# Optimization experiments

Hardware: AMD Instinct MI355X
Metric: run time of the kernel (lower is better)

## Reference

```python
import jax, jax.numpy as jnp
import numpy as np

EPS = 1e-5  # torch InstanceNorm2d default eps


def conv1x1(x, w, b):
    # x: [B,C,H,W], w: [O,C], b: [O]
    return jnp.einsum('bchw,oc->bohw', x, w) + b[None, :, None, None]


def conv3x3(x, w, b):
    y = jax.lax.conv_general_dilated(x, w, (1, 1), 'SAME',
                                     dimension_numbers=('NCHW', 'OIHW', 'NCHW'))
    return y + b[None, :, None, None]


def inorm(x):
    # InstanceNorm2d, affine=False, biased variance
    m = jnp.mean(x, axis=(2, 3), keepdims=True)
    v = jnp.var(x, axis=(2, 3), keepdims=True)
    return (x - m) * jax.lax.rsqrt(v + EPS)


def self_attn(x, wq, bq, wk, bk, wv, bv, gamma):
    B, C, H, W = x.shape
    N = H * W
    q = conv1x1(x, wq, bq).reshape(B, -1, N)   # [B,C/8,N]
    k = conv1x1(x, wk, bk).reshape(B, -1, N)   # [B,C/8,N]
    A = jax.nn.softmax(jnp.einsum('bdn,bdm->bnm', q, k), axis=-1)  # [B,N,N]
    v = conv1x1(x, wv, bv).reshape(B, C, N)    # [B,C,N]
    out = jnp.einsum('bcm,bnm->bcn', v, A).reshape(B, C, H, W)
    return gamma * out + x


def setup_inputs() -> dict:
    key = jax.random.key(0)
    B, C, H, W = 2, 256, 64, 64
    C8 = C // 8
    ks = iter(jax.random.split(key, 40))

    def n(shape, scale=0.05):
        return jax.random.normal(next(ks), shape, dtype=jnp.float32) * scale

    inp = {
        'x': jax.random.normal(next(ks), (B, C, H, W), dtype=jnp.float32),
        'y': jax.random.normal(next(ks), (B, C, H, W), dtype=jnp.float32),
    }
    for p in ('sa1', 'sa2', 'top'):
        inp[p + '_wq'] = n((C8, C)); inp[p + '_bq'] = n((C8,))
        inp[p + '_wk'] = n((C8, C)); inp[p + '_bk'] = n((C8,))
        inp[p + '_wv'] = n((C, C));  inp[p + '_bv'] = n((C,))
        inp[p + '_gamma'] = n((1,), 0.1)
    inp['conv1_w'] = n((C, C, 3, 3)); inp['conv1_b'] = n((C,))
    inp['conv2_w'] = n((C, C, 3, 3)); inp['conv2_b'] = n((C,))
    return inp


def reference(x, y,
              sa1_wq, sa1_bq, sa1_wk, sa1_bk, sa1_wv, sa1_bv, sa1_gamma,
              sa2_wq, sa2_bq, sa2_wk, sa2_bk, sa2_wv, sa2_bv, sa2_gamma,
              top_wq, top_bq, top_wk, top_bk, top_wv, top_bv, top_gamma,
              conv1_w, conv1_b, conv2_w, conv2_b):
    out_1 = inorm(self_attn(x, sa1_wq, sa1_bq, sa1_wk, sa1_bk, sa1_wv, sa1_bv, sa1_gamma))
    out_2 = inorm(out_1 + conv3x3(out_1, conv1_w, conv1_b))
    out_3 = inorm(self_attn(y, sa2_wq, sa2_bq, sa2_wk, sa2_bk, sa2_wv, sa2_bv, sa2_gamma))

    B, C, H, W = out_2.shape
    N = H * W
    q = conv1x1(out_2, top_wq, top_bq).reshape(B, -1, N)
    k = conv1x1(out_2, top_wk, top_bk).reshape(B, -1, N)
    A = jax.nn.softmax(jnp.einsum('bdn,bdm->bnm', q, k), axis=-1)
    v = conv1x1(out_3, top_wv, top_bv).reshape(B, C, N)
    out = jnp.einsum('bcm,bnm->bcn', v, A).reshape(B, C, H, W)
    out = top_gamma * out + y
    out = inorm(out)
    out = inorm(out + out_3)
    out_4 = conv3x3(out, conv2_w, conv2_b)
    out = inorm(out + out_4)
    return out
```

## Files before the change

### kernel.cpp

```cpp
#include <hip/hip_runtime.h>
#include <hip/hip_bf16.h>

typedef __hip_bfloat16 bf16;
typedef __attribute__((ext_vector_type(8))) short s8v;
typedef __attribute__((ext_vector_type(4))) short s4v;
typedef __attribute__((ext_vector_type(4))) float f4v;

#define NPIX 4096
#define CDIM 256
#define MN_ELEMS (1 << 20)
#define QKVSTR (320L * NPIX)
#define QKTSTR (64L * NPIX)

#if __has_builtin(__builtin_amdgcn_exp2f)
#define EXP2F(x) __builtin_amdgcn_exp2f(x)
#else
#define EXP2F(x) exp2f(x)
#endif

typedef __attribute__((address_space(1))) const unsigned int g_u32;
typedef __attribute__((address_space(3))) unsigned int l_u32;
__device__ __forceinline__ void glds16(const void* g, void* l) {
  __builtin_amdgcn_global_load_lds((g_u32*)g, (l_u32*)l, 16, 0, 0);
}

__device__ inline s8v ld8(const bf16* p) { return *(const s8v*)p; }
__device__ inline s8v ld8(const float* p) {
  float4 f0 = *(const float4*)p;
  float4 f1 = *(const float4*)(p + 4);
  s8v r; bf16* e = (bf16*)&r;
  e[0] = __float2bfloat16(f0.x); e[1] = __float2bfloat16(f0.y);
  e[2] = __float2bfloat16(f0.z); e[3] = __float2bfloat16(f0.w);
  e[4] = __float2bfloat16(f1.x); e[5] = __float2bfloat16(f1.y);
  e[6] = __float2bfloat16(f1.z); e[7] = __float2bfloat16(f1.w);
  return r;
}

template<int NT>
__global__ __launch_bounds__(256) void fattn_k(
    const bf16* __restrict__ qkt, const bf16* __restrict__ Vg,
    bf16* __restrict__ out)
{
  constexpr int SN  = NT / 32;
  constexpr int NST = NT / 16;
  __shared__ bf16 k_s[128 * 32];
  __shared__ bf16 p_s[4 * NT * 32];
  float* sums = (float*)k_s;

  const int tid = threadIdx.x;
  const int z = blockIdx.z;
  const int w = tid >> 6, lane = tid & 63;
  const int l15 = lane & 15, oct = lane >> 4;
  const int wr = w >> 1, wc = w & 1;
  const int n0 = blockIdx.x * NT, c0 = blockIdx.y * 128;
  const bf16* qk = qkt + (long)z * QKTSTR;
  const bf16* Vz = Vg + (long)z * QKVSTR;
  const int srow = lane >> 2, scol = (lane & 3) * 8;

  const bf16* vb0 = Vz + (long)(c0 + w * 32 + l15) * 4096 + oct * 8;
  const bf16* vb1 = vb0 + 16L * 4096;

  #pragma unroll
  for (int g = 0; g < NT / 64; ++g)
    glds16(qk + (long)(n0 + g * 64 + (w << 4) + srow) * 64 + scol,
           p_s + g * 2048 + w * 512);
  glds16(qk + (long)((w << 4) + srow) * 64 + 32 + scol, k_s + w * 512);
  glds16(qk + (long)(64 + (w << 4) + srow) * 64 + 32 + scol, k_s + 2048 + w * 512);
  __syncthreads();

  s8v qf[SN];
  #pragma unroll
  for (int st = 0; st < SN; ++st)
    qf[st] = *(const s8v*)(p_s + (wr * (NT / 2) + st * 16 + l15) * 32 + oct * 8);
  __syncthreads();

  f4v acc[2][NST];
  #pragma unroll
  for (int i = 0; i < 2; ++i)
    #pragma unroll
    for (int j = 0; j < NST; ++j) acc[i][j] = (f4v){0.f, 0.f, 0.f, 0.f};
  float rs[SN];
  #pragma unroll
  for (int st = 0; st < SN; ++st) rs[st] = 0.f;

  for (int i = 0; i < 32; ++i) {
    s8v vreg[2][4];
    #pragma unroll
    for (int kk = 0; kk < 4; ++kk) {
      vreg[0][kk] = *(const s8v*)(vb0 + (long)i * 128 + kk * 32);
      vreg[1][kk] = *(const s8v*)(vb1 + (long)i * 128 + kk * 32);
    }
    s8v kf[4];
    #pragma unroll
    for (int nt = 0; nt < 4; ++nt)
      kf[nt] = *(const s8v*)(k_s + (wc * 64 + nt * 16 + l15) * 32 + oct * 8);
    #pragma unroll
    for (int st = 0; st < SN; ++st) {
      const int n = wr * (NT / 2) + st * 16 + l15;
      const int sw = ((n >> 1) & 3) << 4;
      f4v sa[4];
      __builtin_amdgcn_s_setprio(1);
      #pragma unroll
      for (int nt = 0; nt < 4; ++nt) {
        f4v zz = (f4v){0.f, 0.f, 0.f, 0.f};
        sa[nt] = __builtin_amdgcn_mfma_f32_16x16x32_bf16(kf[nt], qf[st], zz, 0, 0, 0);
      }
      __builtin_amdgcn_s_setprio(0);
      #pragma unroll
      for (int nt = 0; nt < 4; ++nt) {
        const int kk = wc * 2 + (nt >> 1);
        int byte = kk * (NT * 64) + n * 64 + (nt & 1) * 32 + oct * 8;
        byte ^= sw;
        s4v pk; bf16* pe = (bf16*)&pk;
        float rsum = 0.f;
        #pragma unroll
        for (int r = 0; r < 4; ++r) {
          float e = EXP2F(sa[nt][r]);
          rsum += e;
          pe[r] = __float2bfloat16(e);
        }
        rs[st] += rsum;
        *(s4v*)((char*)p_s + byte) = pk;
      }
    }
    __syncthreads();
    if (i < 31) {
      const int m1 = (i + 1) * 128;
      glds16(qk + (long)(m1 + (w << 4) + srow) * 64 + 32 + scol, k_s + w * 512);
      glds16(qk + (long)(m1 + 64 + (w << 4) + srow) * 64 + 32 + scol, k_s + 2048 + w * 512);
    }
    #pragma unroll
    for (int kk = 0; kk < 4; ++kk) {
      s8v pf[NST];
      #pragma unroll
      for (int nt = 0; nt < NST; ++nt) {
        const int n = nt * 16 + l15;
        int byte = kk * (NT * 64) + n * 64 + oct * 16;
        byte ^= ((n >> 1) & 3) << 4;
        pf[nt] = *(const s8v*)((const char*)p_s + byte);
      }
      __builtin_amdgcn_s_setprio(1);
      #pragma unroll
      for (int st = 0; st < 2; ++st)
        #pragma unroll
        for (int nt = 0; nt < NST; ++nt)
          acc[st][nt] = __builtin_amdgcn_mfma_f32_16x16x32_bf16(vreg[st][kk], pf[nt], acc[st][nt], 0, 0, 0);
      __builtin_amdgcn_s_setprio(0);
    }
    __syncthreads();
  }

  #pragma unroll
  for (int st = 0; st < SN; ++st) {
    rs[st] += __shfl_xor(rs[st], 16);
    rs[st] += __shfl_xor(rs[st], 32);
  }
  if (lane < 16) {
    #pragma unroll
    for (int st = 0; st < SN; ++st)
      sums[wc * NT + wr * (NT / 2) + st * 16 + l15] = rs[st];
  }
  __syncthreads();

  float rinv[NST];
  #pragma unroll
  for (int nt = 0; nt < NST; ++nt) {
    const int n = nt * 16 + l15;
    rinv[nt] = 1.f / (sums[n] + sums[NT + n]);
  }
  bf16* op = out + (long)z * ((long)CDIM * NPIX);
  #pragma unroll
  for (int st = 0; st < 2; ++st) {
    const int gc = c0 + w * 32 + st * 16 + oct * 4;
    #pragma unroll
    for (int nt = 0; nt < NST; ++nt) {
      const int gn = n0 + nt * 16 + l15;
      #pragma unroll
      for (int r = 0; r < 4; ++r)
        op[(long)(gc + r) * NPIX + gn] = __float2bfloat16(acc[st][nt][r] * rinv[nt]);
    }
  }
}

__global__ __launch_bounds__(256) void gemm128(
    const bf16* __restrict__ A, const bf16* __restrict__ Bm,
    bf16* __restrict__ Cp, int N, int K, int nchunk, int nsplit,
    long abat, long bbat)
{
  __shared__ bf16 a_s0[128 * 32], a_s1[128 * 32];
  __shared__ bf16 b_s0[128 * 32], b_s1[128 * 32];
  const int tid = threadIdx.x;
  const int z = blockIdx.z;
  const int bb = z / nsplit, ks = z - bb * nsplit;
  A  += bb * abat;
  Bm += bb * bbat;
  const int w = tid >> 6, lane = tid & 63;
  const int l15 = lane & 15, oct = lane >> 4;
  const int wr = w >> 1, wc = w & 1;
  const int m0 = blockIdx.y * 128, n0 = blockIdx.x * 128;
  const int kc0 = ks * nchunk, kc1 = kc0 + nchunk;

  const int srow = lane >> 2, skoff = (lane & 3) * 8;
  const long aRow0 = (long)(m0 + (w << 4) + srow) * K;
  const long aRow1 = (long)(m0 + ((w + 4) << 4) + srow) * K;
  const long bRow0 = (long)(n0 + (w << 4) + srow) * K;
  const long bRow1 = (long)(n0 + ((w + 4) << 4) + srow) * K;
  const int ldsOff0 = (w) * 512, ldsOff1 = (w + 4) * 512;

  f4v acc[4][4];
  #pragma unroll
  for (int i = 0; i < 4; ++i)
    #pragma unroll
    for (int j = 0; j < 4; ++j) acc[i][j] = (f4v){0.f, 0.f, 0.f, 0.f};

  for (int kc = kc0; kc < kc1; ++kc) {
    const int kb0 = kc * 64 + skoff;
    const int kb1 = kb0 + 32;
    glds16(A + aRow0 + kb0, a_s0 + ldsOff0);
    glds16(A + aRow1 + kb0, a_s0 + ldsOff1);
    glds16(A + aRow0 + kb1, a_s1 + ldsOff0);
    glds16(A + aRow1 + kb1, a_s1 + ldsOff1);
    glds16(Bm + bRow0 + kb0, b_s0 + ldsOff0);
    glds16(Bm + bRow1 + kb0, b_s0 + ldsOff1);
    glds16(Bm + bRow0 + kb1, b_s1 + ldsOff0);
    glds16(Bm + bRow1 + kb1, b_s1 + ldsOff1);
    __syncthreads();
    #pragma unroll
    for (int h = 0; h < 2; ++h) {
      const bf16* as = h ? a_s1 : a_s0;
      const bf16* bs = h ? b_s1 : b_s0;
      s8v af[4], bfv[4];
      #pragma unroll
      for (int st = 0; st < 4; ++st)
        af[st] = *(const s8v*)(as + (wr * 64 + st * 16 + l15) * 32 + oct * 8);
      #pragma unroll
      for (int nt = 0; nt < 4; ++nt)
        bfv[nt] = *(const s8v*)(bs + (wc * 64 + nt * 16 + l15) * 32 + oct * 8);
      #pragma unroll
      for (int st = 0; st < 4; ++st)
        #pragma unroll
        for (int nt = 0; nt < 4; ++nt)
          acc[st][nt] = __builtin_amdgcn_mfma_f32_16x16x32_bf16(af[st], bfv[nt], acc[st][nt], 0, 0, 0);
    }
    __syncthreads();
  }

  bf16* Cz = Cp + (long)z * ((long)gridDim.y * 128) * N;
  #pragma unroll
  for (int st = 0; st < 4; ++st) {
    const int gm = m0 + wr * 64 + st * 16 + oct * 4;
    #pragma unroll
    for (int nt = 0; nt < 4; ++nt) {
      const int gn = n0 + wc * 64 + nt * 16 + l15;
      #pragma unroll
      for (int r = 0; r < 4; ++r)
        Cz[(long)(gm + r) * N + gn] = __float2bfloat16(acc[st][nt][r]);
    }
  }
}

template<int QKT, typename TBe>
__global__ __launch_bounds__(256) void proj_k(
    const float* __restrict__ A, const float* __restrict__ A2,
    const TBe* __restrict__ B1, const TBe* __restrict__ B2,
    const float* __restrict__ bias, const float* __restrict__ bias2,
    bf16* __restrict__ Cm, bf16* __restrict__ qkt,
    int M, int N, int K, long bbat, long cbat, int nchunk)
{
  __shared__ bf16 a_s[64][40];
  __shared__ bf16 b_s[64][40];
  const int tid = threadIdx.x;
  const int z = blockIdx.z, stage = z >> 1, bat = z & 1;
  const float* Au = stage ? A2 : A;
  const float* biasu = stage ? bias2 : bias;
  const TBe* Bm = (stage ? B2 : B1) + bat * bbat;
  Cm += z * cbat;
  if (QKT) qkt += z * QKTSTR;
  const int m0 = blockIdx.y * 64, n0 = blockIdx.x * 64;
  const int w = tid >> 6, lane = tid & 63;
  const int l15 = lane & 15, oct = lane >> 4;

  f4v acc[4];
  #pragma unroll
  for (int i = 0; i < 4; ++i) acc[i] = (f4v){0.f, 0.f, 0.f, 0.f};

  const int a_i0 = tid >> 2, a_i1 = (tid & 3) * 8;
  const int b_i0 = tid >> 3, b_i1 = (tid & 7) * 8;

  s8v pa, pb;
  auto ldA = [&](int kc, s8v& d) {
    if (m0 + a_i0 < M) d = ld8(Au + (long)(m0 + a_i0) * K + kc * 32 + a_i1);
    else d = (s8v){0,0,0,0,0,0,0,0};
  };
  auto ldB = [&](int kc, s8v& d) {
    d = ld8(Bm + (long)(kc * 32 + b_i0) * N + n0 + b_i1);
  };

  ldA(0, pa); ldB(0, pb);
  for (int kc = 0; kc < nchunk; ++kc) {
    *(s8v*)&a_s[a_i0][a_i1] = pa;
    {
      const bf16* e = (const bf16*)&pb;
      #pragma unroll
      for (int j = 0; j < 8; ++j) b_s[b_i1 + j][b_i0] = e[j];
    }
    __syncthreads();
    if (kc + 1 < nchunk) { ldA(kc + 1, pa); ldB(kc + 1, pb); }
    s8v af = *(const s8v*)&a_s[w * 16 + l15][oct * 8];
    #pragma unroll
    for (int nt = 0; nt < 4; ++nt) {
      s8v bfr = *(const s8v*)&b_s[nt * 16 + l15][oct * 8];
      acc[nt] = __builtin_amdgcn_mfma_f32_16x16x32_bf16(af, bfr, acc[nt], 0, 0, 0);
    }
    __syncthreads();
  }
  const int gm_base = m0 + w * 16 + oct * 4;
  #pragma unroll
  for (int nt = 0; nt < 4; ++nt) {
    const int gn = n0 + nt * 16 + l15;
    #pragma unroll
    for (int r = 0; r < 4; ++r) {
      int gm = gm_base + r;
      if (gm < M) {
        float vv = acc[nt][r] + biasu[gm];
        if (QKT && gm < 64) {
          float vv2 = (gm < 32) ? vv * 1.44269504f : vv;
          qkt[(long)gn * 64 + gm] = __float2bfloat16(vv2);
        } else {
          Cm[(long)gm * N + gn] = __float2bfloat16(vv);
        }
      }
    }
  }
}

__global__ __launch_bounds__(256) void reduce_bias_k(
    const bf16* __restrict__ part, const float* __restrict__ bias,
    bf16* __restrict__ out, int nsplit)
{
  const int g8 = (blockIdx.x * 256 + threadIdx.x) * 8;
  const int b = g8 >> 20, i = g8 & (MN_ELEMS - 1);
  const bf16* p0 = part + (long)b * nsplit * MN_ELEMS + i;
  float s[8];
  { s8v v = *(const s8v*)p0; const bf16* e = (const bf16*)&v;
    #pragma unroll
    for (int j = 0; j < 8; ++j) s[j] = __bfloat162float(e[j]); }
  for (int p = 1; p < nsplit; ++p) {
    s8v v = *(const s8v*)(p0 + (long)p * MN_ELEMS); const bf16* e = (const bf16*)&v;
    #pragma unroll
    for (int j = 0; j < 8; ++j) s[j] += __bfloat162float(e[j]);
  }
  float bv = bias[i >> 12];
  s8v o; bf16* eo = (bf16*)&o;
  #pragma unroll
  for (int j = 0; j < 8; ++j) eo[j] = __float2bfloat16(s[j] + bv);
  *(s8v*)(out + g8) = o;
}

__global__ __launch_bounds__(256) void cat_k(
    const float* __restrict__ wq, const float* __restrict__ bq,
    const float* __restrict__ wk, const float* __restrict__ bk,
    const float* __restrict__ wv, const float* __restrict__ bv,
    float* __restrict__ wcat, float* __restrict__ bcat, int M)
{
  int idx = blockIdx.x * 256 + threadIdx.x;
  int total = M << 8;
  if (idx < total) {
    int r = idx >> 8, c = idx & 255;
    float v;
    if (r < 32) v = wq[r * 256 + c];
    else if (r < 64) v = wk[(r - 32) * 256 + c];
    else v = wv[(r - 64) * 256 + c];
    wcat[idx] = v;
  } else if (idx < total + M) {
    int r = idx - total;
    bcat[r] = (r < 32) ? bq[r] : (r < 64) ? bk[r - 32] : bv[r - 64];
  }
}

__global__ __launch_bounds__(256) void cvtw2_k(
    const float* __restrict__ w1, const float* __restrict__ w2,
    bf16* __restrict__ o1, bf16* __restrict__ o2)
{
  const float* in = blockIdx.y ? w2 : w1;
  bf16* out = blockIdx.y ? o2 : o1;
  int idx = blockIdx.x * 256 + threadIdx.x;
  int o = idx / 2304, r = idx % 2304;
  int j = r >> 8, c = r & 255;
  out[idx] = __float2bfloat16(in[(o * 256 + c) * 9 + j]);
}

__global__ __launch_bounds__(256) void im2colT2_k(const bf16* __restrict__ x,
                                                  bf16* __restrict__ colT)
{
  __shared__ bf16 lds[3 * 66 * 66];
  const int tid = threadIdx.x;
  const int h = blockIdx.x, c0 = blockIdx.y * 64;
  x    += (long)blockIdx.z * CDIM * NPIX;
  colT += (long)blockIdx.z * 2304L * NPIX;

  if (tid < 192) {
    int row = tid >> 6, c = tid & 63;
    lds[(row * 66 + 0) * 66 + c] = __float2bfloat16(0.f);
    lds[(row * 66 + 65) * 66 + c] = __float2bfloat16(0.f);
  }
  const int w2 = tid & 31, chi = tid >> 5;
  #pragma unroll
  for (int it = 0; it < 24; ++it) {
    int row = it >> 3, cg = it & 7;
    int c = cg * 8 + chi;
    int hh = h + row - 1;
    unsigned int pix = 0;
    if ((unsigned)hh < 64u)
      pix = *(const unsigned int*)(x + (long)(c0 + c) * 4096 + hh * 64 + w2 * 2);
    const bf16* pp = (const bf16*)&pix;
    lds[(row * 66 + (w2 * 2 + 1)) * 66 + c] = pp[0];
    lds[(row * 66 + (w2 * 2 + 2)) * 66 + c] = pp[1];
  }
  __syncthreads();
  const int cg8 = tid & 7, wq = tid >> 3;
  #pragma unroll
  for (int j = 0; j < 9; ++j) {
    const int dy = j / 3, dx = j % 3;
    #pragma unroll
    for (int half = 0; half < 2; ++half) {
      int w = wq + half * 32;
      s8v v = *(const s8v*)&lds[(dy * 66 + (w + dx)) * 66 + cg8 * 8];
      *(s8v*)(colT + (long)(h * 64 + w) * 2304 + j * 256 + c0 + cg8 * 8) = v;
    }
  }
}

__device__ inline void ld16(const bf16* p, float* v) {
  s8v r0 = *(const s8v*)p, r1 = *(const s8v*)(p + 8);
  const bf16* e0 = (const bf16*)&r0; const bf16* e1 = (const bf16*)&r1;
  #pragma unroll
  for (int j = 0; j < 8; ++j) { v[j] = __bfloat162float(e0[j]); v[8 + j] = __bfloat162float(e1[j]); }
}
__device__ inline void ld16(const float* p, float* v) {
  #pragma unroll
  for (int q = 0; q < 4; ++q) {
    float4 f = *(const float4*)(p + q * 4);
    v[q * 4 + 0] = f.x; v[q * 4 + 1] = f.y; v[q * 4 + 2] = f.z; v[q * 4 + 3] = f.w;
  }
}
__device__ inline void st16(bf16* p, const float* v) {
  s8v o0, o1v; bf16* f0 = (bf16*)&o0; bf16* f1 = (bf16*)&o1v;
  #pragma unroll
  for (int j = 0; j < 8; ++j) { f0[j] = __float2bfloat16(v[j]); f1[j] = __float2bfloat16(v[8 + j]); }
  *(s8v*)p = o0; *(s8v*)(p + 8) = o1v;
}
__device__ inline void st16(float* p, const float* v) {
  #pragma unroll
  for (int q = 0; q < 4; ++q) {
    float4 f; f.x = v[q * 4 + 0]; f.y = v[q * 4 + 1]; f.z = v[q * 4 + 2]; f.w = v[q * 4 + 3];
    *(float4*)(p + q * 4) = f;
  }
}

template<typename TAe, typename TBe, typename TOe, int G>
__global__ __launch_bounds__(256) void inorm_k(
    const TAe* __restrict__ a, const TBe* __restrict__ b,
    const float* __restrict__ g, TOe* __restrict__ out)
{
  __shared__ float red[8];
  const int tid = threadIdx.x;
  const long base = (long)blockIdx.x * NPIX + tid * 16;
  float gv = G ? *g : 1.f;
  float va[16], vbv[16], v[16];
  ld16(a + base, va);
  ld16(b + base, vbv);
  #pragma unroll
  for (int j = 0; j < 16; ++j) v[j] = gv * va[j] + vbv[j];
  float sum = 0.f, sq = 0.f;
  #pragma unroll
  for (int j = 0; j < 16; ++j) { sum += v[j]; sq += v[j] * v[j]; }
  #pragma unroll
  for (int s = 32; s; s >>= 1) { sum += __shfl_xor(sum, s); sq += __shfl_xor(sq, s); }
  if ((tid & 63) == 0) { red[tid >> 6] = sum; red[4 + (tid >> 6)] = sq; }
  __syncthreads();
  sum = red[0] + red[1] + red[2] + red[3];
  sq  = red[4] + red[5] + red[6] + red[7];
  float mean = sum * (1.f / NPIX);
  float var  = fmaxf(sq * (1.f / NPIX) - mean * mean, 0.f);
  float rstd = rsqrtf(var + 1e-5f);
  float o[16];
  #pragma unroll
  for (int j = 0; j < 16; ++j) o[j] = (v[j] - mean) * rstd;
  st16(out + base, o);
}

static const long CN = (long)CDIM * NPIX;

static void attn_core(int nb, bf16* qkv, bf16* qkt, bf16* t0, hipStream_t stream)
{
  fattn_k<64><<<dim3(64, 2, nb), dim3(256), 0, stream>>>(qkt, qkv + 64 * NPIX, t0);
}

static void run_conv(const bf16* src, const bf16* wcvt, const float* cb,
                     bf16* colT, bf16* part, bf16* dst, hipStream_t stream)
{
  dim3 TB(256);
  im2colT2_k<<<dim3(64, 4, 2), TB, 0, stream>>>(src, colT);
  gemm128<<<dim3(32, 2, 8), TB, 0, stream>>>(wcvt, colT, part, NPIX, 2304, 9, 4,
                                             0L, 2304L * NPIX);
  reduce_bias_k<<<dim3(1024), TB, 0, stream>>>(part, cb, dst, 4);
}

extern "C" void kernel_launch(void* const* d_in, const int* in_sizes, int n_in,
                              void* d_out, int out_size, void* d_ws, size_t ws_size,
                              hipStream_t stream)
{
  (void)in_sizes; (void)n_in; (void)out_size; (void)ws_size;
  const float* x = (const float*)d_in[0];
  const float* y = (const float*)d_in[1];
  auto W = [&](int i) { return (const float*)d_in[i]; };

  char* wp = (char*)d_ws;
  auto take = [&](size_t nbytes) { char* p = wp; wp += (nbytes + 255) & ~(size_t)255; return p; };
  bf16*  qkv   = (bf16*)take((size_t)4 * QKVSTR * 2);
  bf16*  qkt   = (bf16*)take((size_t)4 * QKTSTR * 2);
  bf16*  t0    = (bf16*)take((size_t)4 * CN * 2);
  bf16*  u1    = (bf16*)take(2 * CN * 2);
  bf16*  u2    = (bf16*)take(2 * CN * 2);
  bf16*  u3    = (bf16*)take(2 * CN * 2);
  bf16*  u4    = (bf16*)take(2 * CN * 2);
  bf16*  colT  = (bf16*)take((size_t)2 * 2304L * NPIX * 2);
  bf16*  wcvt1 = (bf16*)take((size_t)589824 * 2);
  bf16*  wcvt2 = (bf16*)take((size_t)589824 * 2);
  float* wcat1 = (float*)take((size_t)81920 * 4);
  float* bcat1 = (float*)take(320 * 4);
  float* wcat2 = (float*)take((size_t)81920 * 4);
  float* bcat2 = (float*)take(320 * 4);
  float* wqk   = (float*)take((size_t)16384 * 4);
  float* bqk   = (float*)take(64 * 4);
  bf16*  part  = (bf16*)take((size_t)8 * MN_ELEMS * 2);
  bf16*  cvout = qkv;

  dim3 TB(256);

  cat_k<<<dim3(322), TB, 0, stream>>>(W(2), W(3), W(4), W(5), W(6), W(7), wcat1, bcat1, 320);
  cat_k<<<dim3(322), TB, 0, stream>>>(W(9), W(10), W(11), W(12), W(13), W(14), wcat2, bcat2, 320);
  cat_k<<<dim3(65),  TB, 0, stream>>>(W(16), W(17), W(18), W(19), nullptr, nullptr, wqk, bqk, 64);
  cvtw2_k<<<dim3(2304, 2), TB, 0, stream>>>(W(23), W(25), wcvt1, wcvt2);

  proj_k<1,float><<<dim3(64,5,4), TB, 0, stream>>>(
      wcat1, wcat2, x, y, bcat1, bcat2, qkv, qkt, 320, NPIX, 256, CN, QKVSTR, 8);
  attn_core(4, qkv, qkt, t0, stream);

  inorm_k<bf16,float,bf16,1><<<dim3(512), TB, 0, stream>>>(t0, x, W(8), u1);
  inorm_k<bf16,float,bf16,1><<<dim3(512), TB, 0, stream>>>(t0 + 2 * CN, y, W(15), u3);

  run_conv(u1, wcvt1, W(24), colT, part, cvout, stream);
  inorm_k<bf16,bf16,bf16,0><<<dim3(512), TB, 0, stream>>>(u1, cvout, nullptr, u2);

  proj_k<1,bf16><<<dim3(64,1,2), TB, 0, stream>>>(
      wqk, wqk, u2, u2, bqk, bqk, qkv, qkt, 64, NPIX, 256, CN, QKVSTR, 8);
  proj_k<0,bf16><<<dim3(64,4,2), TB, 0, stream>>>(
      W(20), W(20), u3, u3, W(21), W(21), qkv + 64 * NPIX, qkt, 256, NPIX, 256, CN, QKVSTR, 8);
  attn_core(2, qkv, qkt, t0, stream);
  inorm_k<bf16,float,bf16,1><<<dim3(512), TB, 0, stream>>>(t0, y, W(22), u1);
  inorm_k<bf16,bf16,bf16,0><<<dim3(512), TB, 0, stream>>>(u1, u3, nullptr, u4);
  run_conv(u4, wcvt2, W(26), colT, part, cvout, stream);
  inorm_k<bf16,bf16,float,0><<<dim3(512), TB, 0, stream>>>(u4, cvout, nullptr, (float*)d_out);
}
```

Before: 399.2 us.

## Restructure flash-attention kernel with per-wave key split and register-resident K/Q fragments

The attention kernel drops the shared-memory staging of Q and K tiles and the block-wide barriers inside the key loop. Each wave now reads its Q and K fragments straight from global memory into registers, double-buffering K across a macro-unrolled pair of steps. Waves split the keys by column half and keep P in a private LDS slab, and the two halves are summed through LDS at the end. The channel tile per block becomes a template parameter chosen by batch count, giving more blocks for the two-batch case. The goal is to remove __syncthreads stalls and LDS traffic, at the cost of more global/L2 loads, higher register pressure and an extra reduction step.

New measurement: 418.4 us. 1.05x slower.

```diff
diff --git a/kernel.cpp b/kernel.cpp
--- a/kernel.cpp
+++ b/kernel.cpp
@@ -36,149 +36,130 @@
   return r;
 }
 
-template<int NT>
+#define ATTN_HALF(I, KFC, KFN)                                                \
+  {                                                                           \
+    s8v vfr[NC][2];                                                           \
+    _Pragma("unroll") for (int cst = 0; cst < NC; ++cst)                      \
+      _Pragma("unroll") for (int b = 0; b < 2; ++b)                           \
+        vfr[cst][b] = *(const s8v*)(vp + (long)cst * 65536 + (long)(I) * 128 + b * 32); \
+    _Pragma("unroll") for (int st = 0; st < 4; ++st) {                        \
+      f4v sa[4];                                                              \
+      __builtin_amdgcn_s_setprio(1);                                          \
+      _Pragma("unroll") for (int nt = 0; nt < 4; ++nt) {                      \
+        f4v zz = (f4v){0.f, 0.f, 0.f, 0.f};                                   \
+        sa[nt] = __builtin_amdgcn_mfma_f32_16x16x32_bf16(KFC[nt], qf[st], zz, 0, 0, 0); \
+      }                                                                       \
+      __builtin_amdgcn_s_setprio(0);                                          \
+      _Pragma("unroll") for (int nt = 0; nt < 4; ++nt) {                      \
+        s4v pk; bf16* pe = (bf16*)&pk;                                        \
+        float rsum = 0.f;                                                     \
+        _Pragma("unroll") for (int r = 0; r < 4; ++r) {                       \
+          float e = EXP2F(sa[nt][r]);                                         \
+          rsum += e; pe[r] = __float2bfloat16(e);                             \
+        }                                                                     \
+        rs[st] += rsum;                                                       \
+        *(s4v*)(slab + ((st * 2 + (nt >> 1)) * 4 + ((nt & 1) * 2 + (oct >> 1))) * 256 \
+                + l15 * 16 + (oct & 1) * 8) = pk;                             \
+      }                                                                       \
+    }                                                                         \
+    { const int inx = ((I) + 1) & 31;                                         \
+      _Pragma("unroll") for (int nt = 0; nt < 4; ++nt)                        \
+        KFN[nt] = *(const s8v*)(kp + (long)inx * 8192 + nt * 1024); }         \
+    _Pragma("unroll") for (int b = 0; b < 2; ++b) {                           \
+      s8v pf[4];                                                              \
+      _Pragma("unroll") for (int st = 0; st < 4; ++st)                        \
+        pf[st] = *(const s8v*)(slab + ((st * 2 + b) * 4 + oct) * 256 + l15 * 16); \
+      __builtin_amdgcn_s_setprio(1);                                          \
+      _Pragma("unroll") for (int cst = 0; cst < NC; ++cst)                    \
+        _Pragma("unroll") for (int st = 0; st < 4; ++st)                      \
+          acc[cst][st] = __builtin_amdgcn_mfma_f32_16x16x32_bf16(vfr[cst][b], pf[st], acc[cst][st], 0, 0, 0); \
+      __builtin_amdgcn_s_setprio(0);                                          \
+    }                                                                         \
+  }
+
+template<int CB>
 __global__ __launch_bounds__(256) void fattn_k(
     const bf16* __restrict__ qkt, const bf16* __restrict__ Vg,
     bf16* __restrict__ out)
 {
-  constexpr int SN  = NT / 32;
-  constexpr int NST = NT / 16;
-  __shared__ bf16 k_s[128 * 32];
-  __shared__ bf16 p_s[4 * NT * 32];
-  float* sums = (float*)k_s;
+  constexpr int NC = CB / 32;
+  __shared__ __align__(16) bf16 p_s[4][4096];
+  __shared__ float sums[2][64];
 
   const int tid = threadIdx.x;
   const int z = blockIdx.z;
   const int w = tid >> 6, lane = tid & 63;
   const int l15 = lane & 15, oct = lane >> 4;
   const int wr = w >> 1, wc = w & 1;
-  const int n0 = blockIdx.x * NT, c0 = blockIdx.y * 128;
+  const int n0 = blockIdx.x * 64;
+  const int c0 = blockIdx.y * CB + wr * (CB / 2);
   const bf16* qk = qkt + (long)z * QKTSTR;
   const bf16* Vz = Vg + (long)z * QKVSTR;
-  const int srow = lane >> 2, scol = (lane & 3) * 8;
-
-  const bf16* vb0 = Vz + (long)(c0 + w * 32 + l15) * 4096 + oct * 8;
-  const bf16* vb1 = vb0 + 16L * 4096;
-
-  #pragma unroll
-  for (int g = 0; g < NT / 64; ++g)
-    glds16(qk + (long)(n0 + g * 64 + (w << 4) + srow) * 64 + scol,
-           p_s + g * 2048 + w * 512);
-  glds16(qk + (long)((w << 4) + srow) * 64 + 32 + scol, k_s + w * 512);
-  glds16(qk + (long)(64 + (w << 4) + srow) * 64 + 32 + scol, k_s + 2048 + w * 512);
-  __syncthreads();
-
-  s8v qf[SN];
-  #pragma unroll
-  for (int st = 0; st < SN; ++st)
-    qf[st] = *(const s8v*)(p_s + (wr * (NT / 2) + st * 16 + l15) * 32 + oct * 8);
-  __syncthreads();
-
-  f4v acc[2][NST];
-  #pragma unroll
-  for (int i = 0; i < 2; ++i)
-    #pragma unroll
-    for (int j = 0; j < NST; ++j) acc[i][j] = (f4v){0.f, 0.f, 0.f, 0.f};
-  float rs[SN];
-  #pragma unroll
-  for (int st = 0; st < SN; ++st) rs[st] = 0.f;
-
-  for (int i = 0; i < 32; ++i) {
-    s8v vreg[2][4];
-    #pragma unroll
-    for (int kk = 0; kk < 4; ++kk) {
-      vreg[0][kk] = *(const s8v*)(vb0 + (long)i * 128 + kk * 32);
-      vreg[1][kk] = *(const s8v*)(vb1 + (long)i * 128 + kk * 32);
-    }
-    s8v kf[4];
-    #pragma unroll
-    for (int nt = 0; nt < 4; ++nt)
-      kf[nt] = *(const s8v*)(k_s + (wc * 64 + nt * 16 + l15) * 32 + oct * 8);
-    #pragma unroll
-    for (int st = 0; st < SN; ++st) {
-      const int n = wr * (NT / 2) + st * 16 + l15;
-      const int sw = ((n >> 1) & 3) << 4;
-      f4v sa[4];
-      __builtin_amdgcn_s_setprio(1);
-      #pragma unroll
-      for (int nt = 0; nt < 4; ++nt) {
-        f4v zz = (f4v){0.f, 0.f, 0.f, 0.f};
-        sa[nt] = __builtin_amdgcn_mfma_f32_16x16x32_bf16(kf[nt], qf[st], zz, 0, 0, 0);
-      }
-      __builtin_amdgcn_s_setprio(0);
-      #pragma unroll
-      for (int nt = 0; nt < 4; ++nt) {
-        const int kk = wc * 2 + (nt >> 1);
-        int byte = kk * (NT * 64) + n * 64 + (nt & 1) * 32 + oct * 8;
-        byte ^= sw;
-        s4v pk; bf16* pe = (bf16*)&pk;
-        float rsum = 0.f;
-        #pragma unroll
-        for (int r = 0; r < 4; ++r) {
-          float e = EXP2F(sa[nt][r]);
-          rsum += e;
-          pe[r] = __float2bfloat16(e);
-        }
-        rs[st] += rsum;
-        *(s4v*)((char*)p_s + byte) = pk;
-      }
-    }
-    __syncthreads();
-    if (i < 31) {
-      const int m1 = (i + 1) * 128;
-      glds16(qk + (long)(m1 + (w << 4) + srow) * 64 + 32 + scol, k_s + w * 512);
-      glds16(qk + (long)(m1 + 64 + (w << 4) + srow) * 64 + 32 + scol, k_s + 2048 + w * 512);
-    }
-    #pragma unroll
-    for (int kk = 0; kk < 4; ++kk) {
-      s8v pf[NST];
-      #pragma unroll
-      for (int nt = 0; nt < NST; ++nt) {
-        const int n = nt * 16 + l15;
-        int byte = kk * (NT * 64) + n * 64 + oct * 16;
-        byte ^= ((n >> 1) & 3) << 4;
-        pf[nt] = *(const s8v*)((const char*)p_s + byte);
-      }
-      __builtin_amdgcn_s_setprio(1);
-      #pragma unroll
-      for (int st = 0; st < 2; ++st)
-        #pragma unroll
-        for (int nt = 0; nt < NST; ++nt)
-          acc[st][nt] = __builtin_amdgcn_mfma_f32_16x16x32_bf16(vreg[st][kk], pf[nt], acc[st][nt], 0, 0, 0);
-      __builtin_amdgcn_s_setprio(0);
-    }
-    __syncthreads();
-  }
-
-  #pragma unroll
-  for (int st = 0; st < SN; ++st) {
+  char* slab = (char*)&p_s[w][0];
+
+  s8v qf[4];
+  #pragma unroll
+  for (int st = 0; st < 4; ++st)
+    qf[st] = *(const s8v*)(qk + (long)(n0 + st * 16 + l15) * 64 + oct * 8);
+
+  const bf16* kp = qk + (long)(wc * 64 + l15) * 64 + 32 + oct * 8;
+  const bf16* vp = Vz + (long)(c0 + l15) * 4096 + wc * 64 + oct * 8;
+
+  f4v acc[NC][4];
+  #pragma unroll
+  for (int i = 0; i < NC; ++i)
+    #pragma unroll
+    for (int j = 0; j < 4; ++j) acc[i][j] = (f4v){0.f, 0.f, 0.f, 0.f};
+  float rs[4] = {0.f, 0.f, 0.f, 0.f};
+
+  s8v kfA[4], kfB[4];
+  #pragma unroll
+  for (int nt = 0; nt < 4; ++nt)
+    kfA[nt] = *(const s8v*)(kp + nt * 1024);
+
+  for (int ii = 0; ii < 16; ++ii) {
+    ATTN_HALF(2 * ii,     kfA, kfB)
+    ATTN_HALF(2 * ii + 1, kfB, kfA)
+  }
+
+  #pragma unroll
+  for (int st = 0; st < 4; ++st) {
     rs[st] += __shfl_xor(rs[st], 16);
     rs[st] += __shfl_xor(rs[st], 32);
   }
-  if (lane < 16) {
-    #pragma unroll
-    for (int st = 0; st < SN; ++st)
-      sums[wc * NT + wr * (NT / 2) + st * 16 + l15] = rs[st];
+  if (wr == 0 && lane < 16) {
+    #pragma unroll
+    for (int st = 0; st < 4; ++st) sums[wc][st * 16 + l15] = rs[st];
   }
   __syncthreads();
 
-  float rinv[NST];
-  #pragma unroll
-  for (int nt = 0; nt < NST; ++nt) {
-    const int n = nt * 16 + l15;
-    rinv[nt] = 1.f / (sums[n] + sums[NT + n]);
-  }
-  bf16* op = out + (long)z * ((long)CDIM * NPIX);
-  #pragma unroll
-  for (int st = 0; st < 2; ++st) {
-    const int gc = c0 + w * 32 + st * 16 + oct * 4;
-    #pragma unroll
-    for (int nt = 0; nt < NST; ++nt) {
-      const int gn = n0 + nt * 16 + l15;
-      #pragma unroll
-      for (int r = 0; r < 4; ++r)
-        op[(long)(gc + r) * NPIX + gn] = __float2bfloat16(acc[st][nt][r] * rinv[nt]);
-    }
+  float* red = (float*)&p_s[0][0];
+  if (wc == 1) {
+    #pragma unroll
+    for (int cst = 0; cst < NC; ++cst)
+      #pragma unroll
+      for (int st = 0; st < 4; ++st)
+        *(f4v*)&red[((wr * NC + cst) * 4 + st) * 256 + l15 * 16 + oct * 4] = acc[cst][st];
+  }
+  __syncthreads();
+  if (wc == 0) {
+    float rinv[4];
+    #pragma unroll
+    for (int st = 0; st < 4; ++st)
+      rinv[st] = 1.f / (sums[0][st * 16 + l15] + sums[1][st * 16 + l15]);
+    bf16* op = out + (long)z * ((long)CDIM * NPIX);
+    #pragma unroll
+    for (int cst = 0; cst < NC; ++cst)
+      #pragma unroll
+      for (int st = 0; st < 4; ++st) {
+        f4v o = acc[cst][st] +
+                *(const f4v*)&red[((wr * NC + cst) * 4 + st) * 256 + l15 * 16 + oct * 4];
+        const int gn = n0 + st * 16 + l15;
+        const int gc = c0 + cst * 16 + oct * 4;
+        #pragma unroll
+        for (int r = 0; r < 4; ++r)
+          op[(long)(gc + r) * NPIX + gn] = __float2bfloat16(o[r] * rinv[st]);
+      }
   }
 }
 
@@ -494,7 +475,10 @@
 
 static void attn_core(int nb, bf16* qkv, bf16* qkt, bf16* t0, hipStream_t stream)
 {
-  fattn_k<64><<<dim3(64, 2, nb), dim3(256), 0, stream>>>(qkt, qkv + 64 * NPIX, t0);
+  if (nb == 4)
+    fattn_k<128><<<dim3(64, 2, 4), dim3(256), 0, stream>>>(qkt, qkv + 64 * NPIX, t0);
+  else
+    fattn_k<64><<<dim3(64, 4, 2), dim3(256), 0, stream>>>(qkt, qkv + 64 * NPIX, t0);
 }
 
 static void run_conv(const bf16* src, const bf16* wcvt, const float* cb,
```

## Restructure flash attention with double-buffered K/V LDS staging and channel-block tiling

Applied to the files above, without the earlier changes.

Rewrites the fused attention kernel so that both K and V tiles are staged into LDS through async global-to-LDS loads. The loads are double-buffered and prefetched one 64-key step ahead, replacing V fragments that were read directly from global memory into registers each step. The tile is reorganized so that a block covers 64 query pixels and CB channels, and the channel block size depends on batch count (128 for 4 batches, 64 with more y-blocks for 2) to raise the number of blocks. The cost is more LDS per block and twice as many synchronized loop iterations, which may reduce occupancy.

After: 411.8 us. 3.2% more time.

```diff
diff --git a/kernel.cpp b/kernel.cpp
--- a/kernel.cpp
+++ b/kernel.cpp
@@ -36,86 +36,88 @@
   return r;
 }
 
-template<int NT>
+template<int CB>
 __global__ __launch_bounds__(256) void fattn_k(
     const bf16* __restrict__ qkt, const bf16* __restrict__ Vg,
     bf16* __restrict__ out)
 {
-  constexpr int SN  = NT / 32;
-  constexpr int NST = NT / 16;
-  __shared__ bf16 k_s[128 * 32];
-  __shared__ bf16 p_s[4 * NT * 32];
-  float* sums = (float*)k_s;
+  constexpr int SC = CB / 32;
+  __shared__ bf16 k_s[2][64 * 32];
+  __shared__ bf16 v_s[2][2 * CB * 32];
+  __shared__ bf16 p_s[2 * 64 * 32];
+  __shared__ float sums[2][64];
 
   const int tid = threadIdx.x;
   const int z = blockIdx.z;
   const int w = tid >> 6, lane = tid & 63;
   const int l15 = lane & 15, oct = lane >> 4;
   const int wr = w >> 1, wc = w & 1;
-  const int n0 = blockIdx.x * NT, c0 = blockIdx.y * 128;
+  const int n0 = blockIdx.x * 64;
+  const int c0 = blockIdx.y * CB;
   const bf16* qk = qkt + (long)z * QKTSTR;
   const bf16* Vz = Vg + (long)z * QKVSTR;
   const int srow = lane >> 2, scol = (lane & 3) * 8;
 
-  const bf16* vb0 = Vz + (long)(c0 + w * 32 + l15) * 4096 + oct * 8;
-  const bf16* vb1 = vb0 + 16L * 4096;
-
-  #pragma unroll
-  for (int g = 0; g < NT / 64; ++g)
-    glds16(qk + (long)(n0 + g * 64 + (w << 4) + srow) * 64 + scol,
-           p_s + g * 2048 + w * 512);
-  glds16(qk + (long)((w << 4) + srow) * 64 + 32 + scol, k_s + w * 512);
-  glds16(qk + (long)(64 + (w << 4) + srow) * 64 + 32 + scol, k_s + 2048 + w * 512);
+  auto stageK = [&](int ms, int buf) {
+    glds16(qk + (long)(ms * 64 + w * 16 + srow) * 64 + 32 + scol,
+           &k_s[buf][(w * 16 + srow) * 32 + scol]);
+  };
+  auto stageV = [&](int ms, int buf) {
+    #pragma unroll
+    for (int kk = 0; kk < 2; ++kk)
+      #pragma unroll
+      for (int rg = 0; rg < CB / 64; ++rg)
+        glds16(Vz + (long)(c0 + rg * 64 + w * 16 + srow) * 4096 + ms * 64 + kk * 32 + scol,
+               &v_s[buf][kk * (CB * 32) + (rg * 64 + w * 16 + srow) * 32 + scol]);
+  };
+
+  s8v qf[2];
+  #pragma unroll
+  for (int st = 0; st < 2; ++st)
+    qf[st] = *(const s8v*)(qk + (long)(n0 + wr * 32 + st * 16 + l15) * 64 + oct * 8);
+
+  stageK(0, 0); stageV(0, 0);
+
+  f4v acc[SC][2];
+  #pragma unroll
+  for (int i = 0; i < SC; ++i)
+    #pragma unroll
+    for (int j = 0; j < 2; ++j) acc[i][j] = (f4v){0.f, 0.f, 0.f, 0.f};
+  float rs[2] = {0.f, 0.f};
+
   __syncthreads();
 
-  s8v qf[SN];
-  #pragma unroll
-  for (int st = 0; st < SN; ++st)
-    qf[st] = *(const s8v*)(p_s + (wr * (NT / 2) + st * 16 + l15) * 32 + oct * 8);
-  __syncthreads();
-
-  f4v acc[2][NST];
-  #pragma unroll
-  for (int i = 0; i < 2; ++i)
-    #pragma unroll
-    for (int j = 0; j < NST; ++j) acc[i][j] = (f4v){0.f, 0.f, 0.f, 0.f};
-  float rs[SN];
-  #pragma unroll
-  for (int st = 0; st < SN; ++st) rs[st] = 0.f;
-
-  for (int i = 0; i < 32; ++i) {
-    s8v vreg[2][4];
-    #pragma unroll
-    for (int kk = 0; kk < 4; ++kk) {
-      vreg[0][kk] = *(const s8v*)(vb0 + (long)i * 128 + kk * 32);
-      vreg[1][kk] = *(const s8v*)(vb1 + (long)i * 128 + kk * 32);
-    }
-    s8v kf[4];
-    #pragma unroll
-    for (int nt = 0; nt < 4; ++nt)
-      kf[nt] = *(const s8v*)(k_s + (wc * 64 + nt * 16 + l15) * 32 + oct * 8);
-    #pragma unroll
-    for (int st = 0; st < SN; ++st) {
-      const int n = wr * (NT / 2) + st * 16 + l15;
+  for (int i = 0; i < 64; ++i) {
+    const int cur = i & 1;
+    if (i < 63) { stageK(i + 1, cur ^ 1); stageV(i + 1, cur ^ 1); }
+
+    s8v kf[2];
+    #pragma unroll
+    for (int nt = 0; nt < 2; ++nt)
+      kf[nt] = *(const s8v*)&k_s[cur][(wc * 32 + nt * 16 + l15) * 32 + oct * 8];
+    f4v sa[2][2];
+    __builtin_amdgcn_s_setprio(1);
+    #pragma unroll
+    for (int nt = 0; nt < 2; ++nt)
+      #pragma unroll
+      for (int st = 0; st < 2; ++st) {
+        f4v zz = (f4v){0.f, 0.f, 0.f, 0.f};
+        sa[nt][st] = __builtin_amdgcn_mfma_f32_16x16x32_bf16(kf[nt], qf[st], zz, 0, 0, 0);
+      }
+    __builtin_amdgcn_s_setprio(0);
+    #pragma unroll
+    for (int st = 0; st < 2; ++st) {
+      const int n = wr * 32 + st * 16 + l15;
       const int sw = ((n >> 1) & 3) << 4;
-      f4v sa[4];
-      __builtin_amdgcn_s_setprio(1);
-      #pragma unroll
-      for (int nt = 0; nt < 4; ++nt) {
-        f4v zz = (f4v){0.f, 0.f, 0.f, 0.f};
-        sa[nt] = __builtin_amdgcn_mfma_f32_16x16x32_bf16(kf[nt], qf[st], zz, 0, 0, 0);
-      }
-      __builtin_amdgcn_s_setprio(0);
-      #pragma unroll
-      for (int nt = 0; nt < 4; ++nt) {
-        const int kk = wc * 2 + (nt >> 1);
-        int byte = kk * (NT * 64) + n * 64 + (nt & 1) * 32 + oct * 8;
+      #pragma unroll
+      for (int nt = 0; nt < 2; ++nt) {
+        int byte = wc * 4096 + n * 64 + nt * 32 + oct * 8;
         byte ^= sw;
         s4v pk; bf16* pe = (bf16*)&pk;
         float rsum = 0.f;
         #pragma unroll
         for (int r = 0; r < 4; ++r) {
-          float e = EXP2F(sa[nt][r]);
+          float e = EXP2F(sa[nt][st][r]);
           rsum += e;
           pe[r] = __float2bfloat16(e);
         }
@@ -124,60 +126,60 @@
       }
     }
     __syncthreads();
-    if (i < 31) {
-      const int m1 = (i + 1) * 128;
-      glds16(qk + (long)(m1 + (w << 4) + srow) * 64 + 32 + scol, k_s + w * 512);
-      glds16(qk + (long)(m1 + 64 + (w << 4) + srow) * 64 + 32 + scol, k_s + 2048 + w * 512);
-    }
-    #pragma unroll
-    for (int kk = 0; kk < 4; ++kk) {
-      s8v pf[NST];
-      #pragma unroll
-      for (int nt = 0; nt < NST; ++nt) {
-        const int n = nt * 16 + l15;
-        int byte = kk * (NT * 64) + n * 64 + oct * 16;
+
+    #pragma unroll
+    for (int kk = 0; kk < 2; ++kk) {
+      s8v pf[2], vf[SC];
+      #pragma unroll
+      for (int j = 0; j < 2; ++j) {
+        const int n = wc * 32 + j * 16 + l15;
+        int byte = kk * 4096 + n * 64 + oct * 16;
         byte ^= ((n >> 1) & 3) << 4;
-        pf[nt] = *(const s8v*)((const char*)p_s + byte);
+        pf[j] = *(const s8v*)((const char*)p_s + byte);
       }
+      #pragma unroll
+      for (int st = 0; st < SC; ++st)
+        vf[st] = *(const s8v*)((const char*)&v_s[cur][0] + kk * (CB * 64)
+                               + (wr * (CB / 2) + st * 16 + l15) * 64 + oct * 16);
       __builtin_amdgcn_s_setprio(1);
       #pragma unroll
-      for (int st = 0; st < 2; ++st)
+      for (int st = 0; st < SC; ++st)
         #pragma unroll
-        for (int nt = 0; nt < NST; ++nt)
-          acc[st][nt] = __builtin_amdgcn_mfma_f32_16x16x32_bf16(vreg[st][kk], pf[nt], acc[st][nt], 0, 0, 0);
+        for (int j = 0; j < 2; ++j)
+          acc[st][j] = __builtin_amdgcn_mfma_f32_16x16x32_bf16(vf[st], pf[j], acc[st][j], 0, 0, 0);
       __builtin_amdgcn_s_setprio(0);
     }
     __syncthreads();
   }
 
   #pragma unroll
-  for (int st = 0; st < SN; ++st) {
+  for (int st = 0; st < 2; ++st) {
     rs[st] += __shfl_xor(rs[st], 16);
     rs[st] += __shfl_xor(rs[st], 32);
   }
-  if (lane < 16) {
-    #pragma unroll
-    for (int st = 0; st < SN; ++st)
-      sums[wc * NT + wr * (NT / 2) + st * 16 + l15] = rs[st];
+  if (oct == 0) {
+    #pragma unroll
+    for (int st = 0; st < 2; ++st)
+      sums[wc][wr * 32 + st * 16 + l15] = rs[st];
   }
   __syncthreads();
 
-  float rinv[NST];
-  #pragma unroll
-  for (int nt = 0; nt < NST; ++nt) {
-    const int n = nt * 16 + l15;
-    rinv[nt] = 1.f / (sums[n] + sums[NT + n]);
+  float rinv[2];
+  #pragma unroll
+  for (int j = 0; j < 2; ++j) {
+    const int n = wc * 32 + j * 16 + l15;
+    rinv[j] = 1.f / (sums[0][n] + sums[1][n]);
   }
   bf16* op = out + (long)z * ((long)CDIM * NPIX);
   #pragma unroll
-  for (int st = 0; st < 2; ++st) {
-    const int gc = c0 + w * 32 + st * 16 + oct * 4;
-    #pragma unroll
-    for (int nt = 0; nt < NST; ++nt) {
-      const int gn = n0 + nt * 16 + l15;
+  for (int st = 0; st < SC; ++st) {
+    const int gc = c0 + wr * (CB / 2) + st * 16 + oct * 4;
+    #pragma unroll
+    for (int j = 0; j < 2; ++j) {
+      const int gn = n0 + wc * 32 + j * 16 + l15;
       #pragma unroll
       for (int r = 0; r < 4; ++r)
-        op[(long)(gc + r) * NPIX + gn] = __float2bfloat16(acc[st][nt][r] * rinv[nt]);
+        op[(long)(gc + r) * NPIX + gn] = __float2bfloat16(acc[st][j][r] * rinv[j]);
     }
   }
 }
@@ -494,7 +496,10 @@
 
 static void attn_core(int nb, bf16* qkv, bf16* qkt, bf16* t0, hipStream_t stream)
 {
-  fattn_k<64><<<dim3(64, 2, nb), dim3(256), 0, stream>>>(qkt, qkv + 64 * NPIX, t0);
+  if (nb == 4)
+    fattn_k<128><<<dim3(64, 2, 4), dim3(256), 0, stream>>>(qkt, qkv + 64 * NPIX, t0);
+  else
+    fattn_k<64><<<dim3(64, 4, 2), dim3(256), 0, stream>>>(qkt, qkv + 64 * NPIX, t0);
 }
 
 static void run_conv(const bf16* src, const bf16* wcvt, const float* cb,
```
